# Kernel tuning notes

Hardware: AMD Instinct MI355X
Metric: run time of the kernel (lower is better)

## Reference

```python
import jax, jax.numpy as jnp
import numpy as np

N, E, DIN, DH, DOUT = 50000, 800000, 128, 128, 64


def setup_inputs() -> dict:
    key = jax.random.key(0)
    ks = jax.random.split(key, 10)
    s = 0.05  # keep activations numerically sane
    return {
        "x": jax.random.normal(ks[0], (N, DIN), jnp.float32),
        "edge_index": jax.random.randint(ks[1], (2, E), 0, N, jnp.int64),
        "w_in": jax.random.normal(ks[2], (DIN, DH), jnp.float32) * s,
        "b_in": jnp.zeros((DH,), jnp.float32),
        "w_l0": jax.random.normal(ks[3], (DH, DH), jnp.float32) * s,
        "w_r0": jax.random.normal(ks[4], (DH, DH), jnp.float32) * s,
        "b0": jnp.zeros((DH,), jnp.float32),
        "w_l1": jax.random.normal(ks[5], (DH, DH), jnp.float32) * s,
        "w_r1": jax.random.normal(ks[6], (DH, DH), jnp.float32) * s,
        "b1": jnp.zeros((DH,), jnp.float32),
        "w_l2": jax.random.normal(ks[7], (DH, DOUT), jnp.float32) * s,
        "w_r2": jax.random.normal(ks[8], (DH, DOUT), jnp.float32) * s,
        "b2": jnp.zeros((DOUT,), jnp.float32),
    }


def _sage_conv(x, src, dst, w_l, w_r, b, n_nodes):
    # PyG SAGEConv (mean aggr): out = lin_l(mean_{j in N(i)} x_j) + lin_r(x_i)
    msg = x[src]  # [E, d] gather
    agg = jax.ops.segment_sum(msg, dst, num_segments=n_nodes)
    deg = jax.ops.segment_sum(jnp.ones((src.shape[0],), x.dtype), dst, num_segments=n_nodes)
    agg = agg / jnp.maximum(deg, 1.0)[:, None]  # isolated nodes -> 0
    return agg @ w_l + x @ w_r + b


def reference(x, edge_index, w_in, b_in, w_l0, w_r0, b0, w_l1, w_r1, b1, w_l2, w_r2, b2):
    src, dst = edge_index[0], edge_index[1]
    n = x.shape[0]
    h = x @ w_in + b_in
    inp = h
    h = jax.nn.relu(h)
    # conv 0 (hidden->hidden) + relu + (eval dropout = id) + residual
    h = _sage_conv(h, src, dst, w_l0, w_r0, b0, n)
    h = jax.nn.relu(h) + 0.2 * inp
    # conv 1 (hidden->hidden)
    h = _sage_conv(h, src, dst, w_l1, w_r1, b1, n)
    h = jax.nn.relu(h) + 0.2 * inp
    # conv 2 (hidden->out), no activation/residual
    h = _sage_conv(h, src, dst, w_l2, w_r2, b2, n)
    return jax.nn.log_softmax(h, axis=-1)
```

## Files before the change

### kernel.cpp

```cpp
#include <hip/hip_runtime.h>
#include <stdint.h>

#define NN 50000
#define NE 800000
#define NBIN 196
#define ABLK 196
#define EPB 4082
#define BCAP 6144
#define NRT 3125
#define GRID_G 1024

typedef __attribute__((ext_vector_type(8))) short short8;
typedef __attribute__((ext_vector_type(4))) float floatx4;

__device__ __forceinline__ uint16_t f2bf(float f){
  union { float f; uint32_t u; } c; c.f = f;
  uint32_t u = c.u + 0x7FFFu + ((c.u >> 16) & 1u);
  return (uint16_t)(u >> 16);
}
__device__ __forceinline__ float bflo(uint32_t v){
  union { uint32_t u; float f; } c; c.u = v << 16; return c.f;
}
__device__ __forceinline__ float bfhi(uint32_t v){
  union { uint32_t u; float f; } c; c.u = v & 0xFFFF0000u; return c.f;
}

#define B_HIST ABLK
#define B_PIN 64
#define B_P0  128
#define B_P1  128
#define B_P2  64

__device__ __forceinline__ void pack_one(int idx, const float* __restrict__ wl,
                                         const float* __restrict__ wr,
                                         uint16_t* __restrict__ bp,
                                         int ncolL, int ncolR, int NT){
  int j = idx & 7, lane = (idx >> 3) & 63, rest = idx >> 9;
  int nt = rest % NT, kt = rest / NT;
  int k = kt * 32 + ((lane >> 4) << 3) + j;
  int n = nt * 16 + (lane & 15);
  float v = (n < ncolL) ? wl[k * ncolL + n] : wr[k * ncolR + (n - ncolL)];
  bp[idx] = f2bf(v);
}

__global__ __launch_bounds__(256) void k_prep(const int* __restrict__ ei, int* __restrict__ histC,
                                              const float* __restrict__ w_in,
                                              const float* __restrict__ w_l0, const float* __restrict__ w_r0,
                                              const float* __restrict__ w_l1, const float* __restrict__ w_r1,
                                              const float* __restrict__ w_l2, const float* __restrict__ w_r2,
                                              uint16_t* __restrict__ bpIn, uint16_t* __restrict__ bp0,
                                              uint16_t* __restrict__ bp1, uint16_t* __restrict__ bp2){
  __shared__ int hsh[NBIN];
  int b = blockIdx.x;
  if (b < B_HIST){
    for (int i = threadIdx.x; i < NBIN; i += 256) hsh[i] = 0;
    __syncthreads();
    int base = b * EPB;
    for (int k = threadIdx.x; k < EPB; k += 256){
      int e = base + k;
      if (e < NE) atomicAdd(&hsh[ei[NE + e] >> 8], 1);
    }
    __syncthreads();
    for (int i = threadIdx.x; i < NBIN; i += 256) histC[b * NBIN + i] = hsh[i];
    return;
  }
  b -= B_HIST;
  if (b < B_PIN){ pack_one(b * 256 + threadIdx.x, w_in, w_in, bpIn, 128, 0, 8); return; }
  b -= B_PIN;
  if (b < B_P0){ pack_one(b * 256 + threadIdx.x, w_l0, w_r0, bp0, 128, 128, 16); return; }
  b -= B_P0;
  if (b < B_P1){ pack_one(b * 256 + threadIdx.x, w_l1, w_r1, bp1, 128, 128, 16); return; }
  b -= B_P1;
  pack_one(b * 256 + threadIdx.x, w_l2, w_r2, bp2, 64, 64, 8);
}

__global__ __launch_bounds__(256) void k_scanS1(const int* __restrict__ histC, int* __restrict__ histE,
                                                int* __restrict__ colTot){
  __shared__ int s[256];
  int t = blockIdx.x;
  int b = threadIdx.x;
  int v = (b < ABLK) ? histC[b * NBIN + t] : 0;
  s[b] = v;
  __syncthreads();
  #pragma unroll
  for (int off = 1; off < 256; off <<= 1){
    int u = (b >= off) ? s[b - off] : 0;
    __syncthreads();
    s[b] += u;
    __syncthreads();
  }
  if (b < ABLK) histE[b * NBIN + t] = s[b] - v;
  if (b == ABLK - 1) colTot[t] = s[b];
}

__global__ __launch_bounds__(256) void k_scanS2(const int* __restrict__ colTot, int* __restrict__ binStart){
  __shared__ int s[256];
  int t = threadIdx.x;
  int tot = (t < NBIN) ? colTot[t] : 0;
  s[t] = tot;
  __syncthreads();
  #pragma unroll
  for (int off = 1; off < 256; off <<= 1){
    int u = (t >= off) ? s[t - off] : 0;
    __syncthreads();
    s[t] += u;
    __syncthreads();
  }
  if (t < NBIN) binStart[t] = s[t] - tot;
  if (t == 0) binStart[NBIN] = NE;
}

__global__ __launch_bounds__(256) void k_bin(const int* __restrict__ ei,
                                             const int* __restrict__ histC, const int* __restrict__ histE,
                                             const int* __restrict__ binStart,
                                             uint32_t* __restrict__ pairs){
  __shared__ int loc[NBIN], cur[NBIN], gof[NBIN];
  __shared__ int sc[256];
  __shared__ uint32_t st[EPB];
  int t = threadIdx.x;
  int b = blockIdx.x;
  int cv = (t < NBIN) ? histC[b * NBIN + t] : 0;
  sc[t] = cv;
  __syncthreads();
  #pragma unroll
  for (int off = 1; off < 256; off <<= 1){
    int u = (t >= off) ? sc[t - off] : 0;
    __syncthreads();
    sc[t] += u;
    __syncthreads();
  }
  if (t < NBIN){
    int excl = sc[t] - cv;
    loc[t] = excl;
    cur[t] = excl;
    gof[t] = binStart[t] + histE[b * NBIN + t];
  }
  __syncthreads();
  int base = b * EPB;
  for (int k = t; k < EPB; k += 256){
    int e = base + k;
    if (e < NE){
      int d = ei[NE + e];
      int s0 = ei[e];
      int pos = atomicAdd(&cur[d >> 8], 1);
      st[pos] = (uint32_t)s0 | ((uint32_t)d << 16);
    }
  }
  __syncthreads();
  int cnt = min(EPB, NE - base);
  for (int k = t; k < cnt; k += 256){
    uint32_t v = st[k];
    int bin = (int)(v >> 24);
    pairs[gof[bin] + (k - loc[bin])] = v;
  }
}

__global__ __launch_bounds__(256) void k_lin0(const float* __restrict__ x,
                                              const uint16_t* __restrict__ BpIn, const float* __restrict__ b_in,
                                              const uint16_t* __restrict__ Bp0, const float* __restrict__ b0,
                                              uint16_t* __restrict__ resb, uint16_t* __restrict__ y0,
                                              uint16_t* __restrict__ z0){
  __shared__ uint16_t smA[16 * 136];
  __shared__ uint16_t smB[16 * 136];
  int t = threadIdx.x;
  int lane = t & 63, wave = t >> 6;
  short8 bIn[4][2], bC0[4][4];
  #pragma unroll
  for (int kt = 0; kt < 4; ++kt){
    #pragma unroll
    for (int n = 0; n < 2; ++n)
      bIn[kt][n] = *(const short8*)(BpIn + (size_t)((kt * 8 + wave * 2 + n) * 64 + lane) * 8);
    #pragma unroll
    for (int n = 0; n < 4; ++n)
      bC0[kt][n] = *(const short8*)(Bp0 + (size_t)((kt * 16 + wave * 4 + n) * 64 + lane) * 8);
  }
  int m = lane & 15, quad = lane >> 4;
  int orow = t >> 4, ochunk = t & 15;
  for (int rt = blockIdx.x; rt < NRT; rt += GRID_G){
    int r0 = rt * 16;
    const float* xrow = x + (size_t)(r0 + m) * 128 + quad * 8;
    short8 af[4];
    #pragma unroll
    for (int kt = 0; kt < 4; ++kt){
      float4 p = *(const float4*)(xrow + kt * 32);
      float4 q2 = *(const float4*)(xrow + kt * 32 + 4);
      short8 a;
      a[0] = (short)f2bf(p.x);  a[1] = (short)f2bf(p.y);
      a[2] = (short)f2bf(p.z);  a[3] = (short)f2bf(p.w);
      a[4] = (short)f2bf(q2.x); a[5] = (short)f2bf(q2.y);
      a[6] = (short)f2bf(q2.z); a[7] = (short)f2bf(q2.w);
      af[kt] = a;
    }
    floatx4 accH[2];
    #pragma unroll
    for (int n = 0; n < 2; ++n) accH[n] = (floatx4){0.f, 0.f, 0.f, 0.f};
    #pragma unroll
    for (int kt = 0; kt < 4; ++kt)
      #pragma unroll
      for (int n = 0; n < 2; ++n)
        accH[n] = __builtin_amdgcn_mfma_f32_16x16x32_bf16(af[kt], bIn[kt][n], accH[n], 0, 0, 0);
    __syncthreads();
    #pragma unroll
    for (int n = 0; n < 2; ++n){
      int c = (wave * 2 + n) * 16 + m;
      float bi = b_in[c];
      #pragma unroll
      for (int i = 0; i < 4; ++i){
        float hh = accH[n][i] + bi;
        int row = quad * 4 + i;
        smA[row * 136 + c] = f2bf(fmaxf(hh, 0.f));
        smB[row * 136 + c] = f2bf(0.2f * hh);
      }
    }
    __syncthreads();
    *((uint4*)(resb + (size_t)(r0 + orow) * 128) + ochunk) = *(const uint4*)&smB[orow * 136 + ochunk * 8];
    short8 af2[4];
    #pragma unroll
    for (int kt = 0; kt < 4; ++kt)
      af2[kt] = *(const short8*)&smA[m * 136 + quad * 8 + kt * 32];
    floatx4 acc[4];
    #pragma unroll
    for (int n = 0; n < 4; ++n) acc[n] = (floatx4){0.f, 0.f, 0.f, 0.f};
    #pragma unroll
    for (int kt = 0; kt < 4; ++kt)
      #pragma unroll
      for (int n = 0; n < 4; ++n)
        acc[n] = __builtin_amdgcn_mfma_f32_16x16x32_bf16(af2[kt], bC0[kt][n], acc[n], 0, 0, 0);
    __syncthreads();
    #pragma unroll
    for (int n = 0; n < 4; ++n){
      int c = (wave * 4 + n) * 16 + m;
      #pragma unroll
      for (int i = 0; i < 4; ++i){
        float v = acc[n][i];
        int row = quad * 4 + i;
        if (c < 128) smA[row * 136 + c] = f2bf(v);
        else         smB[row * 136 + (c - 128)] = f2bf(v + b0[c - 128]);
      }
    }
    __syncthreads();
    *((uint4*)(y0 + (size_t)(r0 + orow) * 128) + ochunk) = *(const uint4*)&smA[orow * 136 + ochunk * 8];
    *((uint4*)(z0 + (size_t)(r0 + orow) * 128) + ochunk) = *(const uint4*)&smB[orow * 136 + ochunk * 8];
  }
}

__global__ __launch_bounds__(256) void k_csr(const uint32_t* __restrict__ pairs, const int* __restrict__ binStart,
                                             int* __restrict__ rowp, uint16_t* __restrict__ colx){
  __shared__ uint32_t pl[BCAP];
  __shared__ uint16_t stg[BCAP];
  __shared__ int h[256], sc[256];
  int i = blockIdx.x, t = threadIdx.x;
  int p0 = binStart[i], p1 = binStart[i + 1];
  int cnt = min(p1 - p0, BCAP);
  for (int k = t; k < cnt; k += 256) pl[k] = pairs[p0 + k];
  h[t] = 0;
  __syncthreads();
  for (int k = t; k < cnt; k += 256) atomicAdd(&h[(pl[k] >> 16) & 255], 1);
  __syncthreads();
  int cv = h[t];
  sc[t] = cv;
  __syncthreads();
  #pragma unroll
  for (int off = 1; off < 256; off <<= 1){
    int u = (t >= off) ? sc[t - off] : 0;
    __syncthreads();
    sc[t] += u;
    __syncthreads();
  }
  int excl = sc[t] - cv;
  int n0 = i << 8;
  int nc = min(256, NN - n0);
  if (t < nc) rowp[n0 + t] = p0 + excl;
  if (i == NBIN - 1 && t == 0) rowp[NN] = NE;
  h[t] = excl;
  __syncthreads();
  for (int k = t; k < cnt; k += 256){
    uint32_t v = pl[k];
    int pos = atomicAdd(&h[(v >> 16) & 255], 1);
    stg[pos] = (uint16_t)(v & 0xFFFFu);
  }
  __syncthreads();
  for (int k = t; k < cnt; k += 256) colx[p0 + k] = stg[k];
}

__global__ __launch_bounds__(256) void k_gemm1(const uint16_t* __restrict__ A, const uint16_t* __restrict__ Bp,
                                               const float* __restrict__ bias,
                                               uint16_t* __restrict__ o0, uint16_t* __restrict__ o1){
  __shared__ uint16_t smY[16 * 136];
  __shared__ uint16_t smZ[16 * 136];
  int t = threadIdx.x;
  int lane = t & 63, wave = t >> 6;
  short8 bfrag[4][4];
  #pragma unroll
  for (int kt = 0; kt < 4; ++kt)
    #pragma unroll
    for (int n = 0; n < 4; ++n)
      bfrag[kt][n] = *(const short8*)(Bp + (size_t)((kt * 16 + wave * 4 + n) * 64 + lane) * 8);
  int m = lane & 15, quad = lane >> 4;
  int orow = t >> 4, ochunk = t & 15;
  for (int rt = blockIdx.x; rt < NRT; rt += GRID_G){
    int r0 = rt * 16;
    const uint16_t* arow = A + (size_t)(r0 + m) * 128 + quad * 8;
    short8 af[4];
    #pragma unroll
    for (int kt = 0; kt < 4; ++kt) af[kt] = *(const short8*)(arow + kt * 32);
    floatx4 acc[4];
    #pragma unroll
    for (int n = 0; n < 4; ++n) acc[n] = (floatx4){0.f, 0.f, 0.f, 0.f};
    #pragma unroll
    for (int kt = 0; kt < 4; ++kt)
      #pragma unroll
      for (int n = 0; n < 4; ++n)
        acc[n] = __builtin_amdgcn_mfma_f32_16x16x32_bf16(af[kt], bfrag[kt][n], acc[n], 0, 0, 0);
    __syncthreads();
    #pragma unroll
    for (int n = 0; n < 4; ++n){
      int c = (wave * 4 + n) * 16 + m;
      #pragma unroll
      for (int i = 0; i < 4; ++i){
        float v = acc[n][i];
        int row = quad * 4 + i;
        if (c < 128) smY[row * 136 + c] = f2bf(v);
        else         smZ[row * 136 + (c - 128)] = f2bf(v + bias[c - 128]);
      }
    }
    __syncthreads();
    *((uint4*)(o0 + (size_t)(r0 + orow) * 128) + ochunk) = *(const uint4*)&smY[orow * 136 + ochunk * 8];
    *((uint4*)(o1 + (size_t)(r0 + orow) * 128) + ochunk) = *(const uint4*)&smZ[orow * 136 + ochunk * 8];
  }
}

__global__ __launch_bounds__(256) void k_gemm2(const uint16_t* __restrict__ A, const uint16_t* __restrict__ Bp,
                                               const float* __restrict__ bias,
                                               uint16_t* __restrict__ o0, float* __restrict__ o2){
  __shared__ uint16_t smY[16 * 72];
  __shared__ float smZ[16 * 68];
  int t = threadIdx.x;
  int lane = t & 63, wave = t >> 6;
  short8 bfrag[4][2];
  #pragma unroll
  for (int kt = 0; kt < 4; ++kt)
    #pragma unroll
    for (int n = 0; n < 2; ++n)
      bfrag[kt][n] = *(const short8*)(Bp + (size_t)((kt * 8 + wave * 2 + n) * 64 + lane) * 8);
  int m = lane & 15, quad = lane >> 4;
  for (int rt = blockIdx.x; rt < NRT; rt += GRID_G){
    int r0 = rt * 16;
    const uint16_t* arow = A + (size_t)(r0 + m) * 128 + quad * 8;
    short8 af[4];
    #pragma unroll
    for (int kt = 0; kt < 4; ++kt) af[kt] = *(const short8*)(arow + kt * 32);
    floatx4 acc[2];
    #pragma unroll
    for (int n = 0; n < 2; ++n) acc[n] = (floatx4){0.f, 0.f, 0.f, 0.f};
    #pragma unroll
    for (int kt = 0; kt < 4; ++kt)
      #pragma unroll
      for (int n = 0; n < 2; ++n)
        acc[n] = __builtin_amdgcn_mfma_f32_16x16x32_bf16(af[kt], bfrag[kt][n], acc[n], 0, 0, 0);
    __syncthreads();
    #pragma unroll
    for (int n = 0; n < 2; ++n){
      int c = (wave * 2 + n) * 16 + m;
      #pragma unroll
      for (int i = 0; i < 4; ++i){
        float v = acc[n][i];
        int row = quad * 4 + i;
        if (c < 64) smY[row * 72 + c] = f2bf(v);
        else        smZ[row * 68 + (c - 64)] = v + bias[c - 64];
      }
    }
    __syncthreads();
    if (t < 128){
      int row = t >> 3, chunk = t & 7;
      *((uint4*)(o0 + (size_t)(r0 + row) * 64) + chunk) = *(const uint4*)&smY[row * 72 + chunk * 8];
    }
    {
      int row = t >> 4, chunk = t & 15;
      *((uint4*)(o2 + (size_t)(r0 + row) * 64) + chunk) = *(const uint4*)&smZ[row * 68 + chunk * 4];
    }
  }
}

__global__ __launch_bounds__(256) void agg_mid(const uint4* __restrict__ yb, const uint4* __restrict__ zb,
                                               const uint4* __restrict__ resb,
                                               const uint16_t* __restrict__ colx, const int* __restrict__ rowp,
                                               uint4* __restrict__ hb_out){
  int wid = blockIdx.x * 4 + (threadIdx.x >> 6);
  if (wid >= NN) return;
  int lane = threadIdx.x & 63;
  int q = lane >> 4, sub = lane & 15;
  int e0 = rowp[wid], e1 = rowp[wid + 1];
  float a0 = 0.f, a1 = 0.f, a2 = 0.f, a3 = 0.f, a4 = 0.f, a5 = 0.f, a6 = 0.f, a7 = 0.f;
  int e = e0 + q;
  for (; e + 12 < e1; e += 16){
    uint4 v0 = yb[(size_t)colx[e]      * 16 + sub];
    uint4 v1 = yb[(size_t)colx[e + 4]  * 16 + sub];
    uint4 v2 = yb[(size_t)colx[e + 8]  * 16 + sub];
    uint4 v3 = yb[(size_t)colx[e + 12] * 16 + sub];
    a0 += bflo(v0.x) + bflo(v1.x) + bflo(v2.x) + bflo(v3.x);
    a1 += bfhi(v0.x) + bfhi(v1.x) + bfhi(v2.x) + bfhi(v3.x);
    a2 += bflo(v0.y) + bflo(v1.y) + bflo(v2.y) + bflo(v3.y);
    a3 += bfhi(v0.y) + bfhi(v1.y) + bfhi(v2.y) + bfhi(v3.y);
    a4 += bflo(v0.z) + bflo(v1.z) + bflo(v2.z) + bflo(v3.z);
    a5 += bfhi(v0.z) + bfhi(v1.z) + bfhi(v2.z) + bfhi(v3.z);
    a6 += bflo(v0.w) + bflo(v1.w) + bflo(v2.w) + bflo(v3.w);
    a7 += bfhi(v0.w) + bfhi(v1.w) + bfhi(v2.w) + bfhi(v3.w);
  }
  for (; e < e1; e += 4){
    uint4 v = yb[(size_t)colx[e] * 16 + sub];
    a0 += bflo(v.x); a1 += bfhi(v.x); a2 += bflo(v.y); a3 += bfhi(v.y);
    a4 += bflo(v.z); a5 += bfhi(v.z); a6 += bflo(v.w); a7 += bfhi(v.w);
  }
  #pragma unroll
  for (int off = 16; off < 64; off <<= 1){
    a0 += __shfl_xor(a0, off, 64);
    a1 += __shfl_xor(a1, off, 64);
    a2 += __shfl_xor(a2, off, 64);
    a3 += __shfl_xor(a3, off, 64);
    a4 += __shfl_xor(a4, off, 64);
    a5 += __shfl_xor(a5, off, 64);
    a6 += __shfl_xor(a6, off, 64);
    a7 += __shfl_xor(a7, off, 64);
  }
  int deg = e1 - e0;
  float inv = deg > 0 ? 1.f / (float)deg : 0.f;
  if (q == 0){
    uint4 zv = zb[(size_t)wid * 16 + sub];
    uint4 rv = resb[(size_t)wid * 16 + sub];
    float w0 = fmaxf(a0 * inv + bflo(zv.x), 0.f) + bflo(rv.x);
    float w1 = fmaxf(a1 * inv + bfhi(zv.x), 0.f) + bfhi(rv.x);
    float w2 = fmaxf(a2 * inv + bflo(zv.y), 0.f) + bflo(rv.y);
    float w3 = fmaxf(a3 * inv + bfhi(zv.y), 0.f) + bfhi(rv.y);
    float w4 = fmaxf(a4 * inv + bflo(zv.z), 0.f) + bflo(rv.z);
    float w5 = fmaxf(a5 * inv + bfhi(zv.z), 0.f) + bfhi(rv.z);
    float w6 = fmaxf(a6 * inv + bflo(zv.w), 0.f) + bflo(rv.w);
    float w7 = fmaxf(a7 * inv + bfhi(zv.w), 0.f) + bfhi(rv.w);
    uint4 o;
    o.x = (uint32_t)f2bf(w0) | ((uint32_t)f2bf(w1) << 16);
    o.y = (uint32_t)f2bf(w2) | ((uint32_t)f2bf(w3) << 16);
    o.z = (uint32_t)f2bf(w4) | ((uint32_t)f2bf(w5) << 16);
    o.w = (uint32_t)f2bf(w6) | ((uint32_t)f2bf(w7) << 16);
    hb_out[(size_t)wid * 16 + sub] = o;
  }
}

__global__ __launch_bounds__(256) void agg_out(const uint2* __restrict__ yb2, const float* __restrict__ z2,
                                               const uint16_t* __restrict__ colx, const int* __restrict__ rowp,
                                               float* __restrict__ out){
  int wid = blockIdx.x * 4 + (threadIdx.x >> 6);
  if (wid >= NN) return;
  int lane = threadIdx.x & 63;
  int q = lane >> 4, sub = lane & 15;
  int e0 = rowp[wid], e1 = rowp[wid + 1];
  float a0 = 0.f, a1 = 0.f, a2 = 0.f, a3 = 0.f;
  int e = e0 + q;
  for (; e + 12 < e1; e += 16){
    uint2 v0 = yb2[(size_t)colx[e]      * 16 + sub];
    uint2 v1 = yb2[(size_t)colx[e + 4]  * 16 + sub];
    uint2 v2 = yb2[(size_t)colx[e + 8]  * 16 + sub];
    uint2 v3 = yb2[(size_t)colx[e + 12] * 16 + sub];
    a0 += bflo(v0.x) + bflo(v1.x) + bflo(v2.x) + bflo(v3.x);
    a1 += bfhi(v0.x) + bfhi(v1.x) + bfhi(v2.x) + bfhi(v3.x);
    a2 += bflo(v0.y) + bflo(v1.y) + bflo(v2.y) + bflo(v3.y);
    a3 += bfhi(v0.y) + bfhi(v1.y) + bfhi(v2.y) + bfhi(v3.y);
  }
  for (; e < e1; e += 4){
    uint2 v = yb2[(size_t)colx[e] * 16 + sub];
    a0 += bflo(v.x); a1 += bfhi(v.x); a2 += bflo(v.y); a3 += bfhi(v.y);
  }
  #pragma unroll
  for (int off = 16; off < 64; off <<= 1){
    a0 += __shfl_xor(a0, off, 64);
    a1 += __shfl_xor(a1, off, 64);
    a2 += __shfl_xor(a2, off, 64);
    a3 += __shfl_xor(a3, off, 64);
  }
  int deg = e1 - e0;
  float inv = deg > 0 ? 1.f / (float)deg : 0.f;
  float4 zv = ((const float4*)z2)[(size_t)wid * 16 + sub];
  float v0 = a0 * inv + zv.x;
  float v1 = a1 * inv + zv.y;
  float v2 = a2 * inv + zv.z;
  float v3 = a3 * inv + zv.w;
  float mx = fmaxf(fmaxf(v0, v1), fmaxf(v2, v3));
  #pragma unroll
  for (int off = 1; off < 16; off <<= 1) mx = fmaxf(mx, __shfl_xor(mx, off, 64));
  float sm = __expf(v0 - mx) + __expf(v1 - mx) + __expf(v2 - mx) + __expf(v3 - mx);
  #pragma unroll
  for (int off = 1; off < 16; off <<= 1) sm += __shfl_xor(sm, off, 64);
  if (q == 0){
    float ls = __logf(sm);
    float4 o = make_float4((v0 - mx) - ls, (v1 - mx) - ls, (v2 - mx) - ls, (v3 - mx) - ls);
    ((float4*)out)[(size_t)wid * 16 + sub] = o;
  }
}

extern "C" void kernel_launch(void* const* d_in, const int* in_sizes, int n_in,
                              void* d_out, int out_size, void* d_ws, size_t ws_size,
                              hipStream_t stream){
  const float* x    = (const float*)d_in[0];
  const int*   ei   = (const int*)d_in[1];
  const float* w_in = (const float*)d_in[2];
  const float* b_in = (const float*)d_in[3];
  const float* w_l0 = (const float*)d_in[4];
  const float* w_r0 = (const float*)d_in[5];
  const float* b0   = (const float*)d_in[6];
  const float* w_l1 = (const float*)d_in[7];
  const float* w_r1 = (const float*)d_in[8];
  const float* b1   = (const float*)d_in[9];
  const float* w_l2 = (const float*)d_in[10];
  const float* w_r2 = (const float*)d_in[11];
  const float* b2   = (const float*)d_in[12];
  float* out = (float*)d_out;

  char* ws = (char*)d_ws;
  size_t off = 0;
  auto take = [&](size_t bytes) -> char* {
    char* p = ws + off;
    off = (off + bytes + 1023) & ~(size_t)1023;
    return p;
  };
  uint16_t* hb   = (uint16_t*)take((size_t)NN * 128 * 2);
  uint16_t* resb = (uint16_t*)take((size_t)NN * 128 * 2);
  uint16_t* y0   = (uint16_t*)take((size_t)NN * 128 * 2);
  uint16_t* z0   = (uint16_t*)take((size_t)NN * 128 * 2);
  uint32_t* pairs = (uint32_t*)take((size_t)NE * 4);
  uint16_t* colx  = (uint16_t*)take((size_t)NE * 2);
  int* histC    = (int*)take((size_t)NBIN * ABLK * 4);
  int* histE    = (int*)take((size_t)NBIN * ABLK * 4);
  int* colTot   = (int*)take((size_t)NBIN * 4);
  int* binStart = (int*)take((size_t)(NBIN + 1) * 4);
  int* rowp     = (int*)take((size_t)(NN + 1) * 4);
  uint16_t* BpIn = (uint16_t*)take(128 * 128 * 2);
  uint16_t* Bp0  = (uint16_t*)take(128 * 256 * 2);
  uint16_t* Bp1  = (uint16_t*)take(128 * 256 * 2);
  uint16_t* Bp2  = (uint16_t*)take(128 * 128 * 2);
  uint16_t* y2 = y0;
  float*    z2 = (float*)z0;
  (void)ws_size; (void)in_sizes; (void)n_in; (void)out_size;

  k_prep<<<B_HIST + B_PIN + B_P0 + B_P1 + B_P2, 256, 0, stream>>>(
      ei, histC, w_in, w_l0, w_r0, w_l1, w_r1, w_l2, w_r2, BpIn, Bp0, Bp1, Bp2);

  k_scanS1<<<NBIN, 256, 0, stream>>>(histC, histE, colTot);
  k_scanS2<<<1, 256, 0, stream>>>(colTot, binStart);

  k_lin0<<<GRID_G, 256, 0, stream>>>(x, BpIn, b_in, Bp0, b0, resb, y0, z0);

  k_bin<<<ABLK, 256, 0, stream>>>(ei, histC, histE, binStart, pairs);
  k_csr<<<NBIN, 256, 0, stream>>>(pairs, binStart, rowp, colx);

  agg_mid<<<NN / 4, 256, 0, stream>>>((const uint4*)y0, (const uint4*)z0, (const uint4*)resb,
                                      colx, rowp, (uint4*)hb);
  k_gemm1<<<GRID_G, 256, 0, stream>>>(hb, Bp1, b1, y0, z0);

  agg_mid<<<NN / 4, 256, 0, stream>>>((const uint4*)y0, (const uint4*)z0, (const uint4*)resb,
                                      colx, rowp, (uint4*)hb);
  k_gemm2<<<GRID_G, 256, 0, stream>>>(hb, Bp2, b2, y2, z2);

  agg_out<<<NN / 4, 256, 0, stream>>>((const uint2*)y2, z2, colx, rowp, out);
}
```

Before: 289.1 us.

## Merge edge binning with input projection and reuse gemm1 for conv0

```diff
diff --git a/kernel.cpp b/kernel.cpp
--- a/kernel.cpp
+++ b/kernel.cpp
@@ -110,73 +110,73 @@
   if (t == 0) binStart[NBIN] = NE;
 }
 
-__global__ __launch_bounds__(256) void k_bin(const int* __restrict__ ei,
+#define B_BIN 196
+#define SMSZ 20488
+
+__global__ __launch_bounds__(256) void k_mid(const int* __restrict__ ei,
                                              const int* __restrict__ histC, const int* __restrict__ histE,
                                              const int* __restrict__ binStart,
-                                             uint32_t* __restrict__ pairs){
-  __shared__ int loc[NBIN], cur[NBIN], gof[NBIN];
-  __shared__ int sc[256];
-  __shared__ uint32_t st[EPB];
+                                             uint32_t* __restrict__ pairs,
+                                             const float* __restrict__ x,
+                                             const uint16_t* __restrict__ BpIn, const float* __restrict__ b_in,
+                                             uint16_t* __restrict__ hb, uint16_t* __restrict__ resb){
+  __shared__ __align__(16) char smraw[SMSZ];
   int t = threadIdx.x;
-  int b = blockIdx.x;
-  int cv = (t < NBIN) ? histC[b * NBIN + t] : 0;
-  sc[t] = cv;
-  __syncthreads();
-  #pragma unroll
-  for (int off = 1; off < 256; off <<= 1){
-    int u = (t >= off) ? sc[t - off] : 0;
-    __syncthreads();
-    sc[t] += u;
-    __syncthreads();
-  }
-  if (t < NBIN){
-    int excl = sc[t] - cv;
-    loc[t] = excl;
-    cur[t] = excl;
-    gof[t] = binStart[t] + histE[b * NBIN + t];
-  }
-  __syncthreads();
-  int base = b * EPB;
-  for (int k = t; k < EPB; k += 256){
-    int e = base + k;
-    if (e < NE){
-      int d = ei[NE + e];
-      int s0 = ei[e];
-      int pos = atomicAdd(&cur[d >> 8], 1);
-      st[pos] = (uint32_t)s0 | ((uint32_t)d << 16);
-    }
-  }
-  __syncthreads();
-  int cnt = min(EPB, NE - base);
-  for (int k = t; k < cnt; k += 256){
-    uint32_t v = st[k];
-    int bin = (int)(v >> 24);
-    pairs[gof[bin] + (k - loc[bin])] = v;
-  }
-}
-
-__global__ __launch_bounds__(256) void k_lin0(const float* __restrict__ x,
-                                              const uint16_t* __restrict__ BpIn, const float* __restrict__ b_in,
-                                              const uint16_t* __restrict__ Bp0, const float* __restrict__ b0,
-                                              uint16_t* __restrict__ resb, uint16_t* __restrict__ y0,
-                                              uint16_t* __restrict__ z0){
-  __shared__ uint16_t smA[16 * 136];
-  __shared__ uint16_t smB[16 * 136];
-  int t = threadIdx.x;
+  if (blockIdx.x < B_BIN){
+    int* loc = (int*)smraw;
+    int* cur = loc + NBIN;
+    int* gof = cur + NBIN;
+    int* sc  = gof + NBIN;
+    uint32_t* st = (uint32_t*)(sc + 256);
+    int b = blockIdx.x;
+    int cv = (t < NBIN) ? histC[b * NBIN + t] : 0;
+    sc[t] = cv;
+    __syncthreads();
+    #pragma unroll
+    for (int off = 1; off < 256; off <<= 1){
+      int u = (t >= off) ? sc[t - off] : 0;
+      __syncthreads();
+      sc[t] += u;
+      __syncthreads();
+    }
+    if (t < NBIN){
+      int excl = sc[t] - cv;
+      loc[t] = excl;
+      cur[t] = excl;
+      gof[t] = binStart[t] + histE[b * NBIN + t];
+    }
+    __syncthreads();
+    int base = b * EPB;
+    for (int k = t; k < EPB; k += 256){
+      int e = base + k;
+      if (e < NE){
+        int d = ei[NE + e];
+        int s0 = ei[e];
+        int pos = atomicAdd(&cur[d >> 8], 1);
+        st[pos] = (uint32_t)s0 | ((uint32_t)d << 16);
+      }
+    }
+    __syncthreads();
+    int cnt = min(EPB, NE - base);
+    for (int k = t; k < cnt; k += 256){
+      uint32_t v = st[k];
+      int bin = (int)(v >> 24);
+      pairs[gof[bin] + (k - loc[bin])] = v;
+    }
+    return;
+  }
+  uint16_t* smA = (uint16_t*)smraw;
+  uint16_t* smB = smA + 16 * 136;
   int lane = t & 63, wave = t >> 6;
-  short8 bIn[4][2], bC0[4][4];
-  #pragma unroll
-  for (int kt = 0; kt < 4; ++kt){
+  short8 bIn[4][2];
+  #pragma unroll
+  for (int kt = 0; kt < 4; ++kt)
     #pragma unroll
     for (int n = 0; n < 2; ++n)
       bIn[kt][n] = *(const short8*)(BpIn + (size_t)((kt * 8 + wave * 2 + n) * 64 + lane) * 8);
-    #pragma unroll
-    for (int n = 0; n < 4; ++n)
-      bC0[kt][n] = *(const short8*)(Bp0 + (size_t)((kt * 16 + wave * 4 + n) * 64 + lane) * 8);
-  }
   int m = lane & 15, quad = lane >> 4;
   int orow = t >> 4, ochunk = t & 15;
-  for (int rt = blockIdx.x; rt < NRT; rt += GRID_G){
+  for (int rt = blockIdx.x - B_BIN; rt < NRT; rt += GRID_G){
     int r0 = rt * 16;
     const float* xrow = x + (size_t)(r0 + m) * 128 + quad * 8;
     short8 af[4];
@@ -213,34 +213,8 @@
       }
     }
     __syncthreads();
+    *((uint4*)(hb   + (size_t)(r0 + orow) * 128) + ochunk) = *(const uint4*)&smA[orow * 136 + ochunk * 8];
     *((uint4*)(resb + (size_t)(r0 + orow) * 128) + ochunk) = *(const uint4*)&smB[orow * 136 + ochunk * 8];
-    short8 af2[4];
-    #pragma unroll
-    for (int kt = 0; kt < 4; ++kt)
-      af2[kt] = *(const short8*)&smA[m * 136 + quad * 8 + kt * 32];
-    floatx4 acc[4];
-    #pragma unroll
-    for (int n = 0; n < 4; ++n) acc[n] = (floatx4){0.f, 0.f, 0.f, 0.f};
-    #pragma unroll
-    for (int kt = 0; kt < 4; ++kt)
-      #pragma unroll
-      for (int n = 0; n < 4; ++n)
-        acc[n] = __builtin_amdgcn_mfma_f32_16x16x32_bf16(af2[kt], bC0[kt][n], acc[n], 0, 0, 0);
-    __syncthreads();
-    #pragma unroll
-    for (int n = 0; n < 4; ++n){
-      int c = (wave * 4 + n) * 16 + m;
-      #pragma unroll
-      for (int i = 0; i < 4; ++i){
-        float v = acc[n][i];
-        int row = quad * 4 + i;
-        if (c < 128) smA[row * 136 + c] = f2bf(v);
-        else         smB[row * 136 + (c - 128)] = f2bf(v + b0[c - 128]);
-      }
-    }
-    __syncthreads();
-    *((uint4*)(y0 + (size_t)(r0 + orow) * 128) + ochunk) = *(const uint4*)&smA[orow * 136 + ochunk * 8];
-    *((uint4*)(z0 + (size_t)(r0 + orow) * 128) + ochunk) = *(const uint4*)&smB[orow * 136 + ochunk * 8];
   }
 }
 
@@ -546,10 +520,12 @@
   k_scanS1<<<NBIN, 256, 0, stream>>>(histC, histE, colTot);
   k_scanS2<<<1, 256, 0, stream>>>(colTot, binStart);
 
-  k_lin0<<<GRID_G, 256, 0, stream>>>(x, BpIn, b_in, Bp0, b0, resb, y0, z0);
-
-  k_bin<<<ABLK, 256, 0, stream>>>(ei, histC, histE, binStart, pairs);
+  k_mid<<<B_BIN + GRID_G, 256, 0, stream>>>(ei, histC, histE, binStart, pairs, x,
+                                            BpIn, b_in, hb, resb);
+
   k_csr<<<NBIN, 256, 0, stream>>>(pairs, binStart, rowp, colx);
+
+  k_gemm1<<<GRID_G, 256, 0, stream>>>(hb, Bp0, b0, y0, z0);
 
   agg_mid<<<NN / 4, 256, 0, stream>>>((const uint4*)y0, (const uint4*)z0, (const uint4*)resb,
                                       colx, rowp, (uint4*)hb);
```

After: 290.2 us. About the same (+0.4%).

## Fuse edge binning and input linear into one kernel; recompute bin offsets locally

Applied to the files above, without the earlier changes.

```diff
diff --git a/kernel.cpp b/kernel.cpp
--- a/kernel.cpp
+++ b/kernel.cpp
@@ -93,76 +93,76 @@
   if (b == ABLK - 1) colTot[t] = s[b];
 }
 
-__global__ __launch_bounds__(256) void k_scanS2(const int* __restrict__ colTot, int* __restrict__ binStart){
-  __shared__ int s[256];
+#define B_BIN 196
+#define SMSZ 19712
+
+__global__ __launch_bounds__(256) void k_mid(const int* __restrict__ ei,
+                                             const int* __restrict__ histC, const int* __restrict__ histE,
+                                             const int* __restrict__ colTot,
+                                             uint32_t* __restrict__ pairs,
+                                             const float* __restrict__ x,
+                                             const uint16_t* __restrict__ BpIn, const float* __restrict__ b_in,
+                                             const uint16_t* __restrict__ Bp0, const float* __restrict__ b0,
+                                             uint16_t* __restrict__ resb, uint16_t* __restrict__ y0,
+                                             uint16_t* __restrict__ z0){
+  __shared__ __align__(16) char smraw[SMSZ];
   int t = threadIdx.x;
-  int tot = (t < NBIN) ? colTot[t] : 0;
-  s[t] = tot;
-  __syncthreads();
-  #pragma unroll
-  for (int off = 1; off < 256; off <<= 1){
-    int u = (t >= off) ? s[t - off] : 0;
-    __syncthreads();
-    s[t] += u;
-    __syncthreads();
-  }
-  if (t < NBIN) binStart[t] = s[t] - tot;
-  if (t == 0) binStart[NBIN] = NE;
-}
-
-__global__ __launch_bounds__(256) void k_bin(const int* __restrict__ ei,
-                                             const int* __restrict__ histC, const int* __restrict__ histE,
-                                             const int* __restrict__ binStart,
-                                             uint32_t* __restrict__ pairs){
-  __shared__ int loc[NBIN], cur[NBIN], gof[NBIN];
-  __shared__ int sc[256];
-  __shared__ uint32_t st[EPB];
-  int t = threadIdx.x;
-  int b = blockIdx.x;
-  int cv = (t < NBIN) ? histC[b * NBIN + t] : 0;
-  sc[t] = cv;
-  __syncthreads();
-  #pragma unroll
-  for (int off = 1; off < 256; off <<= 1){
-    int u = (t >= off) ? sc[t - off] : 0;
-    __syncthreads();
-    sc[t] += u;
-    __syncthreads();
-  }
-  if (t < NBIN){
-    int excl = sc[t] - cv;
-    loc[t] = excl;
-    cur[t] = excl;
-    gof[t] = binStart[t] + histE[b * NBIN + t];
-  }
-  __syncthreads();
-  int base = b * EPB;
-  for (int k = t; k < EPB; k += 256){
-    int e = base + k;
-    if (e < NE){
-      int d = ei[NE + e];
-      int s0 = ei[e];
-      int pos = atomicAdd(&cur[d >> 8], 1);
-      st[pos] = (uint32_t)s0 | ((uint32_t)d << 16);
-    }
-  }
-  __syncthreads();
-  int cnt = min(EPB, NE - base);
-  for (int k = t; k < cnt; k += 256){
-    uint32_t v = st[k];
-    int bin = (int)(v >> 24);
-    pairs[gof[bin] + (k - loc[bin])] = v;
-  }
-}
-
-__global__ __launch_bounds__(256) void k_lin0(const float* __restrict__ x,
-                                              const uint16_t* __restrict__ BpIn, const float* __restrict__ b_in,
-                                              const uint16_t* __restrict__ Bp0, const float* __restrict__ b0,
-                                              uint16_t* __restrict__ resb, uint16_t* __restrict__ y0,
-                                              uint16_t* __restrict__ z0){
-  __shared__ uint16_t smA[16 * 136];
-  __shared__ uint16_t smB[16 * 136];
-  int t = threadIdx.x;
+  if (blockIdx.x < B_BIN){
+    int* loc = (int*)smraw;
+    int* cur = loc + NBIN;
+    int* gof = cur + NBIN;
+    int* sc  = gof + NBIN;
+    uint32_t* st = (uint32_t*)(sc + 256);
+    int b = blockIdx.x;
+    int cv = (t < NBIN) ? histC[b * NBIN + t] : 0;
+    sc[t] = cv;
+    __syncthreads();
+    #pragma unroll
+    for (int off = 1; off < 256; off <<= 1){
+      int u = (t >= off) ? sc[t - off] : 0;
+      __syncthreads();
+      sc[t] += u;
+      __syncthreads();
+    }
+    if (t < NBIN){
+      int excl = sc[t] - cv;
+      loc[t] = excl;
+      cur[t] = excl;
+    }
+    __syncthreads();
+    int ct = (t < NBIN) ? colTot[t] : 0;
+    sc[t] = ct;
+    __syncthreads();
+    #pragma unroll
+    for (int off = 1; off < 256; off <<= 1){
+      int u = (t >= off) ? sc[t - off] : 0;
+      __syncthreads();
+      sc[t] += u;
+      __syncthreads();
+    }
+    if (t < NBIN) gof[t] = (sc[t] - ct) + histE[b * NBIN + t];
+    __syncthreads();
+    int base = b * EPB;
+    for (int k = t; k < EPB; k += 256){
+      int e = base + k;
+      if (e < NE){
+        int d = ei[NE + e];
+        int s0 = ei[e];
+        int pos = atomicAdd(&cur[d >> 8], 1);
+        st[pos] = (uint32_t)s0 | ((uint32_t)d << 16);
+      }
+    }
+    __syncthreads();
+    int cnt = min(EPB, NE - base);
+    for (int k = t; k < cnt; k += 256){
+      uint32_t v = st[k];
+      int bin = (int)(v >> 24);
+      pairs[gof[bin] + (k - loc[bin])] = v;
+    }
+    return;
+  }
+  uint16_t* smA = (uint16_t*)smraw;
+  uint16_t* smB = smA + 16 * 136;
   int lane = t & 63, wave = t >> 6;
   short8 bIn[4][2], bC0[4][4];
   #pragma unroll
@@ -176,81 +176,91 @@
   }
   int m = lane & 15, quad = lane >> 4;
   int orow = t >> 4, ochunk = t & 15;
-  for (int rt = blockIdx.x; rt < NRT; rt += GRID_G){
-    int r0 = rt * 16;
-    const float* xrow = x + (size_t)(r0 + m) * 128 + quad * 8;
-    short8 af[4];
-    #pragma unroll
-    for (int kt = 0; kt < 4; ++kt){
-      float4 p = *(const float4*)(xrow + kt * 32);
-      float4 q2 = *(const float4*)(xrow + kt * 32 + 4);
-      short8 a;
-      a[0] = (short)f2bf(p.x);  a[1] = (short)f2bf(p.y);
-      a[2] = (short)f2bf(p.z);  a[3] = (short)f2bf(p.w);
-      a[4] = (short)f2bf(q2.x); a[5] = (short)f2bf(q2.y);
-      a[6] = (short)f2bf(q2.z); a[7] = (short)f2bf(q2.w);
-      af[kt] = a;
-    }
-    floatx4 accH[2];
-    #pragma unroll
-    for (int n = 0; n < 2; ++n) accH[n] = (floatx4){0.f, 0.f, 0.f, 0.f};
-    #pragma unroll
-    for (int kt = 0; kt < 4; ++kt)
-      #pragma unroll
-      for (int n = 0; n < 2; ++n)
-        accH[n] = __builtin_amdgcn_mfma_f32_16x16x32_bf16(af[kt], bIn[kt][n], accH[n], 0, 0, 0);
-    __syncthreads();
-    #pragma unroll
-    for (int n = 0; n < 2; ++n){
-      int c = (wave * 2 + n) * 16 + m;
-      float bi = b_in[c];
-      #pragma unroll
-      for (int i = 0; i < 4; ++i){
-        float hh = accH[n][i] + bi;
-        int row = quad * 4 + i;
-        smA[row * 136 + c] = f2bf(fmaxf(hh, 0.f));
-        smB[row * 136 + c] = f2bf(0.2f * hh);
-      }
-    }
-    __syncthreads();
-    *((uint4*)(resb + (size_t)(r0 + orow) * 128) + ochunk) = *(const uint4*)&smB[orow * 136 + ochunk * 8];
-    short8 af2[4];
-    #pragma unroll
-    for (int kt = 0; kt < 4; ++kt)
-      af2[kt] = *(const short8*)&smA[m * 136 + quad * 8 + kt * 32];
-    floatx4 acc[4];
-    #pragma unroll
-    for (int n = 0; n < 4; ++n) acc[n] = (floatx4){0.f, 0.f, 0.f, 0.f};
-    #pragma unroll
-    for (int kt = 0; kt < 4; ++kt)
-      #pragma unroll
-      for (int n = 0; n < 4; ++n)
-        acc[n] = __builtin_amdgcn_mfma_f32_16x16x32_bf16(af2[kt], bC0[kt][n], acc[n], 0, 0, 0);
-    __syncthreads();
-    #pragma unroll
-    for (int n = 0; n < 4; ++n){
-      int c = (wave * 4 + n) * 16 + m;
-      #pragma unroll
-      for (int i = 0; i < 4; ++i){
-        float v = acc[n][i];
-        int row = quad * 4 + i;
-        if (c < 128) smA[row * 136 + c] = f2bf(v);
-        else         smB[row * 136 + (c - 128)] = f2bf(v + b0[c - 128]);
-      }
-    }
-    __syncthreads();
-    *((uint4*)(y0 + (size_t)(r0 + orow) * 128) + ochunk) = *(const uint4*)&smA[orow * 136 + ochunk * 8];
-    *((uint4*)(z0 + (size_t)(r0 + orow) * 128) + ochunk) = *(const uint4*)&smB[orow * 136 + ochunk * 8];
-  }
-}
-
-__global__ __launch_bounds__(256) void k_csr(const uint32_t* __restrict__ pairs, const int* __restrict__ binStart,
+  int r0 = (blockIdx.x - B_BIN) * 16;
+  const float* xrow = x + (size_t)(r0 + m) * 128 + quad * 8;
+  short8 af[4];
+  #pragma unroll
+  for (int kt = 0; kt < 4; ++kt){
+    float4 p = *(const float4*)(xrow + kt * 32);
+    float4 q2 = *(const float4*)(xrow + kt * 32 + 4);
+    short8 a;
+    a[0] = (short)f2bf(p.x);  a[1] = (short)f2bf(p.y);
+    a[2] = (short)f2bf(p.z);  a[3] = (short)f2bf(p.w);
+    a[4] = (short)f2bf(q2.x); a[5] = (short)f2bf(q2.y);
+    a[6] = (short)f2bf(q2.z); a[7] = (short)f2bf(q2.w);
+    af[kt] = a;
+  }
+  floatx4 accH[2];
+  #pragma unroll
+  for (int n = 0; n < 2; ++n) accH[n] = (floatx4){0.f, 0.f, 0.f, 0.f};
+  #pragma unroll
+  for (int kt = 0; kt < 4; ++kt)
+    #pragma unroll
+    for (int n = 0; n < 2; ++n)
+      accH[n] = __builtin_amdgcn_mfma_f32_16x16x32_bf16(af[kt], bIn[kt][n], accH[n], 0, 0, 0);
+  #pragma unroll
+  for (int n = 0; n < 2; ++n){
+    int c = (wave * 2 + n) * 16 + m;
+    float bi = b_in[c];
+    #pragma unroll
+    for (int i = 0; i < 4; ++i){
+      float hh = accH[n][i] + bi;
+      int row = quad * 4 + i;
+      smA[row * 136 + c] = f2bf(fmaxf(hh, 0.f));
+      smB[row * 136 + c] = f2bf(0.2f * hh);
+    }
+  }
+  __syncthreads();
+  *((uint4*)(resb + (size_t)(r0 + orow) * 128) + ochunk) = *(const uint4*)&smB[orow * 136 + ochunk * 8];
+  short8 af2[4];
+  #pragma unroll
+  for (int kt = 0; kt < 4; ++kt)
+    af2[kt] = *(const short8*)&smA[m * 136 + quad * 8 + kt * 32];
+  floatx4 acc[4];
+  #pragma unroll
+  for (int n = 0; n < 4; ++n) acc[n] = (floatx4){0.f, 0.f, 0.f, 0.f};
+  #pragma unroll
+  for (int kt = 0; kt < 4; ++kt)
+    #pragma unroll
+    for (int n = 0; n < 4; ++n)
+      acc[n] = __builtin_amdgcn_mfma_f32_16x16x32_bf16(af2[kt], bC0[kt][n], acc[n], 0, 0, 0);
+  __syncthreads();
+  #pragma unroll
+  for (int n = 0; n < 4; ++n){
+    int c = (wave * 4 + n) * 16 + m;
+    #pragma unroll
+    for (int i = 0; i < 4; ++i){
+      float v = acc[n][i];
+      int row = quad * 4 + i;
+      if (c < 128) smA[row * 136 + c] = f2bf(v);
+      else         smB[row * 136 + (c - 128)] = f2bf(v + b0[c - 128]);
+    }
+  }
+  __syncthreads();
+  *((uint4*)(y0 + (size_t)(r0 + orow) * 128) + ochunk) = *(const uint4*)&smA[orow * 136 + ochunk * 8];
+  *((uint4*)(z0 + (size_t)(r0 + orow) * 128) + ochunk) = *(const uint4*)&smB[orow * 136 + ochunk * 8];
+}
+
+__global__ __launch_bounds__(256) void k_csr(const uint32_t* __restrict__ pairs, const int* __restrict__ colTot,
                                              int* __restrict__ rowp, uint16_t* __restrict__ colx){
   __shared__ uint32_t pl[BCAP];
   __shared__ uint16_t stg[BCAP];
   __shared__ int h[256], sc[256];
+  __shared__ int sp0, sp1;
   int i = blockIdx.x, t = threadIdx.x;
-  int p0 = binStart[i], p1 = binStart[i + 1];
+  int ct = (t < NBIN) ? colTot[t] : 0;
+  sc[t] = ct;
+  __syncthreads();
+  #pragma unroll
+  for (int off = 1; off < 256; off <<= 1){
+    int u = (t >= off) ? sc[t - off] : 0;
+    __syncthreads();
+    sc[t] += u;
+    __syncthreads();
+  }
+  if (t == i){ sp0 = sc[t] - ct; sp1 = sc[t]; }
+  __syncthreads();
+  int p0 = sp0, p1 = sp1;
   int cnt = min(p1 - p0, BCAP);
   for (int k = t; k < cnt; k += 256) pl[k] = pairs[p0 + k];
   h[t] = 0;
@@ -530,7 +540,6 @@
   int* histC    = (int*)take((size_t)NBIN * ABLK * 4);
   int* histE    = (int*)take((size_t)NBIN * ABLK * 4);
   int* colTot   = (int*)take((size_t)NBIN * 4);
-  int* binStart = (int*)take((size_t)(NBIN + 1) * 4);
   int* rowp     = (int*)take((size_t)(NN + 1) * 4);
   uint16_t* BpIn = (uint16_t*)take(128 * 128 * 2);
   uint16_t* Bp0  = (uint16_t*)take(128 * 256 * 2);
@@ -544,12 +553,11 @@
       ei, histC, w_in, w_l0, w_r0, w_l1, w_r1, w_l2, w_r2, BpIn, Bp0, Bp1, Bp2);
 
   k_scanS1<<<NBIN, 256, 0, stream>>>(histC, histE, colTot);
-  k_scanS2<<<1, 256, 0, stream>>>(colTot, binStart);
-
-  k_lin0<<<GRID_G, 256, 0, stream>>>(x, BpIn, b_in, Bp0, b0, resb, y0, z0);
-
-  k_bin<<<ABLK, 256, 0, stream>>>(ei, histC, histE, binStart, pairs);
-  k_csr<<<NBIN, 256, 0, stream>>>(pairs, binStart, rowp, colx);
+
+  k_mid<<<B_BIN + NRT, 256, 0, stream>>>(ei, histC, histE, colTot, pairs, x,
+                                         BpIn, b_in, Bp0, b0, resb, y0, z0);
+
+  k_csr<<<NBIN, 256, 0, stream>>>(pairs, colTot, rowp, colx);
 
   agg_mid<<<NN / 4, 256, 0, stream>>>((const uint4*)y0, (const uint4*)z0, (const uint4*)resb,
                                       colx, rowp, (uint4*)hb);
```

Measured after the change: 277.0 us. 4.2% less time.
